# Optimization experiments

Hardware: AMD Instinct MI355X
Metric: run time of the kernel (lower is better)

The kernel has to match this reference:

```python
import jax, jax.numpy as jnp
import numpy as np

N_HEADS = 12
NEG_INF = -1e9


def rotate_half(x):
    x1, x2 = jnp.split(x, 2, axis=-1)
    return jnp.concatenate((-x2, x1), axis=-1)


def rope_tables(T, D, dtype):
    # matches RotaryEmbedding buffers: emb = cat(freqs, freqs), shape [1,1,T,D]
    inv_freq = 1.0 / (10000.0 ** (jnp.arange(0, D, 2, dtype=jnp.float32) / D))
    t = jnp.arange(T, dtype=jnp.float32)
    freqs = jnp.einsum('i,j->ij', t, inv_freq)
    emb = jnp.concatenate((freqs, freqs), axis=-1)
    return jnp.cos(emb)[None, None].astype(dtype), jnp.sin(emb)[None, None].astype(dtype)


def setup_inputs() -> dict:
    key = jax.random.key(0)
    ks = jax.random.split(key, 5)
    B, T, C = 4, 2048, 768
    s = 1.0 / np.sqrt(C)
    x = jax.random.normal(ks[0], (B, T, C), dtype=jnp.float32)
    wq = jax.random.normal(ks[1], (C, C), dtype=jnp.float32) * s
    wk = jax.random.normal(ks[2], (C, C), dtype=jnp.float32) * s
    wv = jax.random.normal(ks[3], (C, C), dtype=jnp.float32) * s
    wo = jax.random.normal(ks[4], (C, C), dtype=jnp.float32) * s
    causal = jnp.tril(jnp.ones((T, T), dtype=bool))
    mask = jnp.where(causal, 0.0, NEG_INF).astype(jnp.float32)[None, None]
    return {"x": x, "wq": wq, "wk": wk, "wv": wv, "wo": wo, "mask": mask}


def reference(x, wq, wk, wv, wo, mask):
    B, T, C = x.shape
    H = N_HEADS
    D = C // H
    # QKV projections (no bias), reshape to [B,H,T,D]
    def proj(w):
        return (x @ w).reshape(B, T, H, D).transpose(0, 2, 1, 3)
    q, k, v = proj(wq), proj(wk), proj(wv)
    cos, sin = rope_tables(T, D, x.dtype)
    q = q * cos + rotate_half(q) * sin
    k = k * cos + rotate_half(k) * sin
    attn = jnp.einsum('bhqd,bhkd->bhqk', q, k) / jnp.sqrt(jnp.asarray(D, x.dtype))
    attn = attn + mask
    attn = jax.nn.softmax(attn, axis=-1)  # dropout = identity (eval mode)
    out = jnp.einsum('bhqk,bhkd->bhqd', attn, v)
    out = out.transpose(0, 2, 1, 3).reshape(B, T, C)
    return out @ wo
```

## Files before the change

### kernel.cpp

```cpp
#include <hip/hip_runtime.h>
#include <hip/hip_bf16.h>
#include <cmath>

typedef _Float16 f16x8 __attribute__((ext_vector_type(8)));
typedef float f32x4 __attribute__((ext_vector_type(4)));

#define T_SEQ 2048
#define C_DIM 768
#define H_NUM 12
#define NX (8192 * 768)
#define NW (768 * 768)

__device__ __forceinline__ unsigned short f2h(float f) {
    _Float16 h = (_Float16)f;
    return __builtin_bit_cast(unsigned short, h);
}

__device__ __forceinline__ float fexp2(float x) {
#if __has_builtin(__builtin_amdgcn_exp2f)
    return __builtin_amdgcn_exp2f(x);
#else
    return exp2f(x);
#endif
}

__device__ __forceinline__ unsigned int pkrtz(float a, float b) {
    auto r = __builtin_amdgcn_cvt_pkrtz(a, b);
    return __builtin_bit_cast(unsigned int, r);
}

__device__ __forceinline__ unsigned int permlo(unsigned int d0, unsigned int d1) {
#if __has_builtin(__builtin_amdgcn_perm)
    return __builtin_amdgcn_perm(d1, d0, 0x05040100u);
#else
    return (d0 & 0xffffu) | (d1 << 16);
#endif
}
__device__ __forceinline__ unsigned int permhi(unsigned int d0, unsigned int d1) {
#if __has_builtin(__builtin_amdgcn_perm)
    return __builtin_amdgcn_perm(d1, d0, 0x07060302u);
#else
    return (d0 >> 16) | (d1 & 0xffff0000u);
#endif
}

__device__ __forceinline__ void gld16(const unsigned short* g, unsigned short* l) {
    __builtin_amdgcn_global_load_lds(
        (const __attribute__((address_space(1))) unsigned int*)g,
        (__attribute__((address_space(3))) unsigned int*)l, 16, 0, 0);
}

__global__ __launch_bounds__(256)
void prep(const float* __restrict__ x,
          const float* __restrict__ w0, const float* __restrict__ w1,
          const float* __restrict__ w2, const float* __restrict__ w3,
          unsigned short* __restrict__ xb, unsigned short* __restrict__ wt) {
    __shared__ float T[64][65];
    const int pid = blockIdx.x;
    if (pid < 3072) {
        int cidx = pid * 256 + threadIdx.x;
        int row = cidx / 96;
        int cp = cidx - row * 96;
        int dchunk = row * 96 + (cp & ~3) + ((cp & 3) ^ (row & 3));
        const float* s = x + (size_t)cidx * 8;
        float4 v0 = *(const float4*)s, v1 = *(const float4*)(s + 4);
        ushort4 a, b;
        a.x = f2h(v0.x); a.y = f2h(v0.y); a.z = f2h(v0.z); a.w = f2h(v0.w);
        b.x = f2h(v1.x); b.y = f2h(v1.y); b.z = f2h(v1.z); b.w = f2h(v1.w);
        unsigned short* d = xb + (size_t)dchunk * 8;
        *(ushort4*)d = a;
        *(ushort4*)(d + 4) = b;
    } else {
        int t = pid - 3072;
        int z = t / 144, r = t - z * 144;
        int kx = r / 12, ny = r - kx * 12;
        const float* src = (z == 0) ? w0 : (z == 1) ? w1 : (z == 2) ? w2 : w3;
        unsigned short* dst = wt + (size_t)z * NW;
        const int k0 = kx * 64, n0 = ny * 64;
        const int tid = threadIdx.x;
        {
            int rowb = tid >> 4, c4 = (tid & 15) * 4;
#pragma unroll
            for (int i = 0; i < 4; ++i) {
                int row = rowb + i * 16;
                float4 v = *(const float4*)&src[(size_t)(k0 + row) * C_DIM + n0 + c4];
                T[row][c4] = v.x; T[row][c4 + 1] = v.y; T[row][c4 + 2] = v.z; T[row][c4 + 3] = v.w;
            }
        }
        __syncthreads();
        {
            int n = tid & 63, kseg = (tid >> 6) * 16;
            int n_glob = n0 + n;
            unsigned short tmp[16];
#pragma unroll
            for (int j = 0; j < 16; ++j) tmp[j] = f2h(T[kseg + j][n]);
            int base = k0 + (kseg & 32);
            int sub = (kseg >> 3) & 3;
            unsigned short* drow = dst + (size_t)n_glob * C_DIM + base;
            *(uint4*)&drow[(sub ^ (n_glob & 3)) << 3]       = *(uint4*)&tmp[0];
            *(uint4*)&drow[((sub + 1) ^ (n_glob & 3)) << 3] = *(uint4*)&tmp[8];
        }
    }
}

__global__ __launch_bounds__(256, 4)
void qkv_gemm(const unsigned short* __restrict__ xb,
              const unsigned short* __restrict__ wt,
              unsigned short* __restrict__ q_ws,
              unsigned short* __restrict__ k_ws,
              unsigned short* __restrict__ vt_ws) {
    const int pid = blockIdx.x;
    const int xcd = pid & 7, idx = pid >> 3;
    const int mloc = idx / 18, nw = idx - mloc * 18;
    const int which = nw % 3, nx = nw / 3;
    const unsigned short* W = wt + (size_t)which * NW;
    const int n0 = nx * 128, m0 = (xcd * 8 + mloc) * 128;

    __shared__ __align__(16) unsigned short As[8192];
    __shared__ __align__(16) unsigned short Bs[8192];

    const int tid = threadIdx.x, lane = tid & 63, w = tid >> 6;
    const int quad = lane >> 4, l16 = lane & 15;
    const int wm = (w >> 1) * 64, wn = (w & 1) * 64;

    f32x4 acc[4][4] = {};

    for (int k0 = 0; k0 < C_DIM; k0 += 64) {
        __syncthreads();
#pragma unroll
        for (int c = 0; c < 4; ++c) {
            int e = c * 256 + tid;
            int p = e >> 9, row = (e >> 2) & 127, ch = e & 3;
            int kc = k0 + p * 32 + ch * 8;
            gld16(xb + (size_t)(m0 + row) * C_DIM + kc, &As[e * 8]);
            gld16(W  + (size_t)(n0 + row) * C_DIM + kc, &Bs[e * 8]);
        }
        __syncthreads();
#pragma unroll
        for (int p = 0; p < 2; ++p) {
            f16x8 af[4], bf[4];
#pragma unroll
            for (int mt = 0; mt < 4; ++mt) {
                int r = wm + mt * 16 + l16;
                af[mt] = *(const f16x8*)&As[p * 4096 + r * 32 + ((quad ^ (r & 3)) << 3)];
            }
#pragma unroll
            for (int nt = 0; nt < 4; ++nt) {
                int r = wn + nt * 16 + l16;
                bf[nt] = *(const f16x8*)&Bs[p * 4096 + r * 32 + ((quad ^ (r & 3)) << 3)];
            }
#pragma unroll
            for (int mt = 0; mt < 4; ++mt)
#pragma unroll
                for (int nt = 0; nt < 4; ++nt)
                    acc[mt][nt] = __builtin_amdgcn_mfma_f32_16x16x32_f16(af[mt], bf[nt], acc[mt][nt], 0, 0, 0);
        }
    }

    const int head = nx * 2 + (w & 1);

    if (which < 2) {
        unsigned short* dst = (which == 0) ? q_ws : k_ws;
        const float qscale = 0.18033688011112042f;
#pragma unroll
        for (int ntp = 0; ntp < 2; ++ntp) {
            int d1 = ntp * 16 + l16;
            float invf = __expf(-0.28782313662425572f * (float)d1);
#pragma unroll
            for (int mt = 0; mt < 4; ++mt)
#pragma unroll
                for (int reg = 0; reg < 4; ++reg) {
                    int m = m0 + wm + mt * 16 + quad * 4 + reg;
                    int t = m & (T_SEQ - 1), bb = m >> 11;
                    float sn, cs;
                    __sincosf((float)t * invf, &sn, &cs);
                    float v1 = acc[mt][ntp][reg], v2 = acc[mt][ntp + 2][reg];
                    float o1 = v1 * cs - v2 * sn;
                    float o2 = v2 * cs + v1 * sn;
                    if (which == 0) { o1 *= qscale; o2 *= qscale; }
                    size_t o = ((size_t)(bb * H_NUM + head) * T_SEQ + t) * 64 + d1;
                    dst[o] = f2h(o1);
                    dst[o + 32] = f2h(o2);
                }
        }
    } else {
#pragma unroll
        for (int nt = 0; nt < 4; ++nt) {
            int d = nt * 16 + l16;
#pragma unroll
            for (int mt = 0; mt < 4; ++mt) {
                int m = m0 + wm + mt * 16 + quad * 4;
                int t = m & (T_SEQ - 1), bb = m >> 11;
                ushort4 pk;
                pk.x = f2h(acc[mt][nt][0]); pk.y = f2h(acc[mt][nt][1]);
                pk.z = f2h(acc[mt][nt][2]); pk.w = f2h(acc[mt][nt][3]);
                *(ushort4*)&vt_ws[((size_t)(bb * H_NUM + head) * 64 + d) * T_SEQ + t] = pk;
            }
        }
    }
}

__global__ __launch_bounds__(256, 3)
void flash_attn(const unsigned short* __restrict__ q_ws,
                const unsigned short* __restrict__ k_ws,
                const unsigned short* __restrict__ vt_ws,
                unsigned short* __restrict__ attn_out) {
    __shared__ __align__(16) unsigned short Kbuf[2][64 * 64];
    __shared__ __align__(16) unsigned short Vbuf[2][64 * 64];
    __shared__ __align__(16) unsigned int Ps32[4][16 * 64];

    const int pid = blockIdx.x;
    const int xcd = pid & 7, slot = pid >> 3;
    const int bh_l = slot >> 4;
    const int bh = xcd * 6 + bh_l;
    const int pr = (slot + 3 * bh_l) & 15;
    const int qa = pr, qb = 31 - pr;
    const int b = bh / H_NUM, h = bh % H_NUM;

    const int tid = threadIdx.x, lane = tid & 63, w = tid >> 6;
    const int quad = lane >> 4, l16 = lane & 15;
    const size_t base = (size_t)bh * (T_SEQ * 64);

    const unsigned short* qAp = q_ws + base + (size_t)(qa * 64 + w * 16 + l16) * 64 + quad * 8;
    f16x8 aqA0 = *(const f16x8*)(qAp);
    f16x8 aqA1 = *(const f16x8*)(qAp + 32);
    const unsigned short* qBp = q_ws + base + (size_t)(qb * 64 + w * 16 + l16) * 64 + quad * 8;
    f16x8 aqB0 = *(const f16x8*)(qBp);
    f16x8 aqB1 = *(const f16x8*)(qBp + 32);

    f32x4 accA[4] = {}, accB[4] = {};
    f32x4 laccA = {}, laccB = {};
    f16x8 onesf;
#pragma unroll
    for (int i = 0; i < 8; ++i) onesf[i] = (_Float16)1.0f;

    unsigned int* pw = &Ps32[w][0];

    const int r_in = lane >> 3;
    const int cpr = lane & 7;
    const int gch = (cpr ^ r_in) * 8;

#define DMA_KV(P, KT)                                                                  \
    {                                                                                  \
        _Pragma("unroll")                                                              \
        for (int j = 0; j < 2; ++j) {                                                  \
            int row = w * 16 + j * 8 + r_in;                                           \
            gld16(k_ws + base + (size_t)((KT) * 64 + row) * 64 + gch,                  \
                  &Kbuf[P][(w * 16 + j * 8) * 64]);                                    \
            gld16(vt_ws + base + (size_t)row * T_SEQ + (KT) * 64 + gch,                \
                  &Vbuf[P][(w * 16 + j * 8) * 64]);                                    \
        }                                                                              \
    }

    const int fo = (quad ^ (l16 & 7)) << 3;

    const int wg = (quad & 1) * 4;
    const int l16q = l16 >> 2, l16m = l16 & 3;
    const int s7 = l16 & 7;
    const int rA = l16 * 64;
    const int rp0a = rA + (((2 * quad) ^ s7) << 2);
    const int rp0b = rA + (((2 * quad + 1) ^ s7) << 2);

    DMA_KV(0, 0);
    for (int kt = 0; kt <= qb; ++kt) {
        const int cur = kt & 1;
        __syncthreads();
        if (kt < qb) DMA_KV(cur ^ 1, kt + 1);
        const int doA = (kt <= qa);

        f16x8 bk[4][2], bv[4][2];
#pragma unroll
        for (int nt = 0; nt < 4; ++nt) {
            const unsigned short* kr = &Kbuf[cur][(nt * 16 + l16) * 64 + fo];
            bk[nt][0] = *(const f16x8*)(kr);
            bk[nt][1] = *(const f16x8*)((const unsigned short*)((size_t)kr ^ 64));
            const unsigned short* vr = &Vbuf[cur][(nt * 16 + l16) * 64 + fo];
            bv[nt][0] = *(const f16x8*)(vr);
            bv[nt][1] = *(const f16x8*)((const unsigned short*)((size_t)vr ^ 64));
        }

        f32x4 sB[4] = {}, sA[4] = {};
        __builtin_amdgcn_s_setprio(1);
#pragma unroll
        for (int nt = 0; nt < 4; ++nt) {
            sB[nt] = __builtin_amdgcn_mfma_f32_16x16x32_f16(aqB0, bk[nt][0], sB[nt], 0, 0, 0);
            sB[nt] = __builtin_amdgcn_mfma_f32_16x16x32_f16(aqB1, bk[nt][1], sB[nt], 0, 0, 0);
        }
        if (doA) {
#pragma unroll
            for (int nt = 0; nt < 4; ++nt) {
                sA[nt] = __builtin_amdgcn_mfma_f32_16x16x32_f16(aqA0, bk[nt][0], sA[nt], 0, 0, 0);
                sA[nt] = __builtin_amdgcn_mfma_f32_16x16x32_f16(aqA1, bk[nt][1], sA[nt], 0, 0, 0);
            }
        }
        __builtin_amdgcn_s_setprio(0);
        if (kt == qb) {
#pragma unroll
            for (int nt = 0; nt < 4; ++nt)
#pragma unroll
                for (int reg = 0; reg < 4; ++reg)
                    if (nt * 16 + l16 > w * 16 + quad * 4 + reg) sB[nt][reg] = -1e30f;
        }
        if (kt == qa) {
#pragma unroll
            for (int nt = 0; nt < 4; ++nt)
#pragma unroll
                for (int reg = 0; reg < 4; ++reg)
                    if (nt * 16 + l16 > w * 16 + quad * 4 + reg) sA[nt][reg] = -1e30f;
        }

        if (doA) {
#pragma unroll
            for (int nt = 0; nt < 4; ++nt)
#pragma unroll
                for (int reg = 0; reg < 4; ++reg) {
                    float pB = fexp2(sB[nt][reg]);
                    float pA = fexp2(sA[nt][reg]);
                    pw[(quad * 4 + reg) * 64 + ((((nt * 4) | l16q) ^ (wg | reg)) << 2) + l16m] = pkrtz(pB, pA);
                }
        } else {
#pragma unroll
            for (int nt = 0; nt < 4; ++nt)
#pragma unroll
                for (int reg = 0; reg < 4; ++reg) {
                    float pB = fexp2(sB[nt][reg]);
                    pw[(quad * 4 + reg) * 64 + ((((nt * 4) | l16q) ^ (wg | reg)) << 2) + l16m] = pkrtz(pB, pB);
                }
        }

        uint4 c0 = *(const uint4*)(pw + rp0a);
        uint4 c1 = *(const uint4*)(pw + rp0b);
        uint4 c2 = *(const uint4*)(pw + rp0a + 32);
        uint4 c3 = *(const uint4*)(pw + rp0b + 32);

        uint4 lo0 = { permlo(c0.x, c0.y), permlo(c0.z, c0.w), permlo(c1.x, c1.y), permlo(c1.z, c1.w) };
        uint4 lo1 = { permlo(c2.x, c2.y), permlo(c2.z, c2.w), permlo(c3.x, c3.y), permlo(c3.z, c3.w) };
        f16x8 apB0 = __builtin_bit_cast(f16x8, lo0);
        f16x8 apB1 = __builtin_bit_cast(f16x8, lo1);
        __builtin_amdgcn_s_setprio(1);
#pragma unroll
        for (int nt = 0; nt < 4; ++nt) {
            accB[nt] = __builtin_amdgcn_mfma_f32_16x16x32_f16(apB0, bv[nt][0], accB[nt], 0, 0, 0);
            accB[nt] = __builtin_amdgcn_mfma_f32_16x16x32_f16(apB1, bv[nt][1], accB[nt], 0, 0, 0);
        }
        laccB = __builtin_amdgcn_mfma_f32_16x16x32_f16(apB0, onesf, laccB, 0, 0, 0);
        laccB = __builtin_amdgcn_mfma_f32_16x16x32_f16(apB1, onesf, laccB, 0, 0, 0);
        __builtin_amdgcn_s_setprio(0);
        if (doA) {
            uint4 hi0 = { permhi(c0.x, c0.y), permhi(c0.z, c0.w), permhi(c1.x, c1.y), permhi(c1.z, c1.w) };
            uint4 hi1 = { permhi(c2.x, c2.y), permhi(c2.z, c2.w), permhi(c3.x, c3.y), permhi(c3.z, c3.w) };
            f16x8 apA0 = __builtin_bit_cast(f16x8, hi0);
            f16x8 apA1 = __builtin_bit_cast(f16x8, hi1);
            __builtin_amdgcn_s_setprio(1);
#pragma unroll
            for (int nt = 0; nt < 4; ++nt) {
                accA[nt] = __builtin_amdgcn_mfma_f32_16x16x32_f16(apA0, bv[nt][0], accA[nt], 0, 0, 0);
                accA[nt] = __builtin_amdgcn_mfma_f32_16x16x32_f16(apA1, bv[nt][1], accA[nt], 0, 0, 0);
            }
            laccA = __builtin_amdgcn_mfma_f32_16x16x32_f16(apA0, onesf, laccA, 0, 0, 0);
            laccA = __builtin_amdgcn_mfma_f32_16x16x32_f16(apA1, onesf, laccA, 0, 0, 0);
            __builtin_amdgcn_s_setprio(0);
        }
    }
#undef DMA_KV

    float lB[4], lA[4];
#pragma unroll
    for (int reg = 0; reg < 4; ++reg) {
        lB[reg] = 1.0f / laccB[reg];
        lA[reg] = 1.0f / laccA[reg];
    }
#pragma unroll
    for (int nt = 0; nt < 4; ++nt)
#pragma unroll
        for (int reg = 0; reg < 4; ++reg) {
            int col = h * 64 + nt * 16 + l16;
            int tB = qb * 64 + w * 16 + quad * 4 + reg;
            attn_out[(size_t)(b * T_SEQ + tB) * C_DIM + col] = f2h(accB[nt][reg] * lB[reg]);
            int tA = qa * 64 + w * 16 + quad * 4 + reg;
            attn_out[(size_t)(b * T_SEQ + tA) * C_DIM + col] = f2h(accA[nt][reg] * lA[reg]);
        }
}

__global__ __launch_bounds__(256, 3)
void out_proj(const unsigned short* __restrict__ ab,
              const unsigned short* __restrict__ wt_o,
              float* __restrict__ out) {
    const int pid = blockIdx.x;
    const int xcd = pid & 7, idx = pid >> 3;
    const int mloc = idx / 6, nx = idx - mloc * 6;
    const int n0 = nx * 128, m0 = (xcd * 8 + mloc) * 128;

    __shared__ __align__(16) unsigned short As[8192];
    __shared__ __align__(16) unsigned short Bs[8192];

    const int tid = threadIdx.x, lane = tid & 63, w = tid >> 6;
    const int quad = lane >> 4, l16 = lane & 15;
    const int wm = (w >> 1) * 64, wn = (w & 1) * 64;

    f32x4 acc[4][4] = {};
    const int srow = tid >> 1, shalf = tid & 1;

    for (int k0 = 0; k0 < C_DIM; k0 += 64) {
        __syncthreads();
#pragma unroll
        for (int p = 0; p < 2; ++p) {
            const unsigned short* g = ab + (size_t)(m0 + srow) * C_DIM + k0 + p * 32 + shalf * 16;
            uint4 d0 = *(const uint4*)g;
            uint4 d1 = *(const uint4*)(g + 8);
            *(uint4*)&As[p * 4096 + srow * 32 + (((shalf * 2 + 0) ^ (srow & 3)) << 3)] = d0;
            *(uint4*)&As[p * 4096 + srow * 32 + (((shalf * 2 + 1) ^ (srow & 3)) << 3)] = d1;
        }
#pragma unroll
        for (int c = 0; c < 4; ++c) {
            int e = c * 256 + tid;
            int p = e >> 9, row = (e >> 2) & 127, ch = e & 3;
            gld16(wt_o + (size_t)(n0 + row) * C_DIM + k0 + p * 32 + ch * 8, &Bs[e * 8]);
        }
        __syncthreads();
#pragma unroll
        for (int p = 0; p < 2; ++p) {
            f16x8 af[4], bf[4];
#pragma unroll
            for (int mt = 0; mt < 4; ++mt) {
                int r = wm + mt * 16 + l16;
                af[mt] = *(const f16x8*)&As[p * 4096 + r * 32 + ((quad ^ (r & 3)) << 3)];
            }
#pragma unroll
            for (int nt = 0; nt < 4; ++nt) {
                int r = wn + nt * 16 + l16;
                bf[nt] = *(const f16x8*)&Bs[p * 4096 + r * 32 + ((quad ^ (r & 3)) << 3)];
            }
#pragma unroll
            for (int mt = 0; mt < 4; ++mt)
#pragma unroll
                for (int nt = 0; nt < 4; ++nt)
                    acc[mt][nt] = __builtin_amdgcn_mfma_f32_16x16x32_f16(af[mt], bf[nt], acc[mt][nt], 0, 0, 0);
        }
    }

#pragma unroll
    for (int mt = 0; mt < 4; ++mt)
#pragma unroll
        for (int nt = 0; nt < 4; ++nt)
#pragma unroll
            for (int reg = 0; reg < 4; ++reg) {
                int m = m0 + wm + mt * 16 + quad * 4 + reg;
                int n = n0 + wn + nt * 16 + l16;
                out[(size_t)m * C_DIM + n] = acc[mt][nt][reg];
            }
}

extern "C" void kernel_launch(void* const* d_in, const int* in_sizes, int n_in,
                              void* d_out, int out_size, void* d_ws, size_t ws_size,
                              hipStream_t stream) {
    const float* x  = (const float*)d_in[0];
    const float* wq = (const float*)d_in[1];
    const float* wk = (const float*)d_in[2];
    const float* wv = (const float*)d_in[3];
    const float* wo = (const float*)d_in[4];
    float* out = (float*)d_out;

    unsigned short* xb    = (unsigned short*)d_ws;
    unsigned short* wt    = xb + NX;
    unsigned short* q_ws  = wt + 4 * (size_t)NW;
    unsigned short* k_ws  = q_ws + NX;
    unsigned short* vt_ws = k_ws + NX;
    unsigned short* attn  = xb;

    prep<<<3648, 256, 0, stream>>>(x, wq, wk, wv, wo, xb, wt);
    qkv_gemm<<<1152, 256, 0, stream>>>(xb, wt, q_ws, k_ws, vt_ws);
    flash_attn<<<768, 256, 0, stream>>>(q_ws, k_ws, vt_ws, attn);
    out_proj<<<384, 256, 0, stream>>>(attn, wt + 3 * (size_t)NW, out);
}
```

Measured before the change: 222.3 us.

## Compute transposed scores so P stays in registers, removing LDS round-trip

The QK^T MFMA now swaps its operands to produce S^T, so each lane's exponentiated probabilities already sit in the B-operand layout a 16x16x16 MFMA needs for the PV product. This removes the per-wave LDS staging buffer for P, along with its writes, reads and perm repacking. The row-sum moves from ones-vector MFMAs to fdot2 accumulation plus cross-lane shuffles at the end. V fragments are now read from LDS with 8-byte loads inside the PV loop, and PV uses twice as many smaller MFMAs. The output is written with vectorized ushort4 stores.

New measurement: 213.5 us. -4.0%, faster.

```diff
diff --git a/kernel.cpp b/kernel.cpp
--- a/kernel.cpp
+++ b/kernel.cpp
@@ -3,7 +3,9 @@
 #include <cmath>
 
 typedef _Float16 f16x8 __attribute__((ext_vector_type(8)));
+typedef _Float16 f16x4 __attribute__((ext_vector_type(4)));
 typedef float f32x4 __attribute__((ext_vector_type(4)));
+using h2_t = decltype(__builtin_amdgcn_cvt_pkrtz(0.f, 0.f));
 
 #define T_SEQ 2048
 #define C_DIM 768
@@ -24,23 +26,18 @@
 #endif
 }
 
-__device__ __forceinline__ unsigned int pkrtz(float a, float b) {
-    auto r = __builtin_amdgcn_cvt_pkrtz(a, b);
-    return __builtin_bit_cast(unsigned int, r);
-}
-
-__device__ __forceinline__ unsigned int permlo(unsigned int d0, unsigned int d1) {
-#if __has_builtin(__builtin_amdgcn_perm)
-    return __builtin_amdgcn_perm(d1, d0, 0x05040100u);
+__device__ __forceinline__ f16x4 mk4(h2_t a, h2_t b) {
+    uint2 u;
+    u.x = __builtin_bit_cast(unsigned int, a);
+    u.y = __builtin_bit_cast(unsigned int, b);
+    return __builtin_bit_cast(f16x4, u);
+}
+
+__device__ __forceinline__ float dot2acc(h2_t d, h2_t o, float acc) {
+#if __has_builtin(__builtin_amdgcn_fdot2)
+    return __builtin_amdgcn_fdot2(d, o, acc, false);
 #else
-    return (d0 & 0xffffu) | (d1 << 16);
-#endif
-}
-__device__ __forceinline__ unsigned int permhi(unsigned int d0, unsigned int d1) {
-#if __has_builtin(__builtin_amdgcn_perm)
-    return __builtin_amdgcn_perm(d1, d0, 0x07060302u);
-#else
-    return (d0 >> 16) | (d1 & 0xffff0000u);
+    return acc + (float)d[0] + (float)d[1];
 #endif
 }
 
@@ -207,7 +204,6 @@
                 unsigned short* __restrict__ attn_out) {
     __shared__ __align__(16) unsigned short Kbuf[2][64 * 64];
     __shared__ __align__(16) unsigned short Vbuf[2][64 * 64];
-    __shared__ __align__(16) unsigned int Ps32[4][16 * 64];
 
     const int pid = blockIdx.x;
     const int xcd = pid & 7, slot = pid >> 3;
@@ -229,12 +225,8 @@
     f16x8 aqB1 = *(const f16x8*)(qBp + 32);
 
     f32x4 accA[4] = {}, accB[4] = {};
-    f32x4 laccA = {}, laccB = {};
-    f16x8 onesf;
-#pragma unroll
-    for (int i = 0; i < 8; ++i) onesf[i] = (_Float16)1.0f;
-
-    unsigned int* pw = &Ps32[w][0];
+    float laccA = 0.f, laccB = 0.f;
+    const h2_t ones2 = __builtin_amdgcn_cvt_pkrtz(1.f, 1.f);
 
     const int r_in = lane >> 3;
     const int cpr = lane & 7;
@@ -254,12 +246,11 @@
 
     const int fo = (quad ^ (l16 & 7)) << 3;
 
-    const int wg = (quad & 1) * 4;
-    const int l16q = l16 >> 2, l16m = l16 & 3;
-    const int s7 = l16 & 7;
-    const int rA = l16 * 64;
-    const int rp0a = rA + (((2 * quad) ^ s7) << 2);
-    const int rp0b = rA + (((2 * quad + 1) ^ s7) << 2);
+    const int q1 = quad >> 1, q0 = quad & 1, s7 = l16 & 7;
+    int voff[4];
+#pragma unroll
+    for (int kb = 0; kb < 4; ++kb)
+        voff[kb] = (((((kb << 1) | q1) ^ s7) << 3) | (q0 << 2));
 
     DMA_KV(0, 0);
     for (int kt = 0; kt <= qb; ++kt) {
@@ -268,118 +259,113 @@
         if (kt < qb) DMA_KV(cur ^ 1, kt + 1);
         const int doA = (kt <= qa);
 
-        f16x8 bk[4][2], bv[4][2];
+        f16x8 bk[4][2];
 #pragma unroll
         for (int nt = 0; nt < 4; ++nt) {
             const unsigned short* kr = &Kbuf[cur][(nt * 16 + l16) * 64 + fo];
             bk[nt][0] = *(const f16x8*)(kr);
             bk[nt][1] = *(const f16x8*)((const unsigned short*)((size_t)kr ^ 64));
-            const unsigned short* vr = &Vbuf[cur][(nt * 16 + l16) * 64 + fo];
-            bv[nt][0] = *(const f16x8*)(vr);
-            bv[nt][1] = *(const f16x8*)((const unsigned short*)((size_t)vr ^ 64));
         }
 
         f32x4 sB[4] = {}, sA[4] = {};
         __builtin_amdgcn_s_setprio(1);
 #pragma unroll
         for (int nt = 0; nt < 4; ++nt) {
-            sB[nt] = __builtin_amdgcn_mfma_f32_16x16x32_f16(aqB0, bk[nt][0], sB[nt], 0, 0, 0);
-            sB[nt] = __builtin_amdgcn_mfma_f32_16x16x32_f16(aqB1, bk[nt][1], sB[nt], 0, 0, 0);
+            sB[nt] = __builtin_amdgcn_mfma_f32_16x16x32_f16(bk[nt][0], aqB0, sB[nt], 0, 0, 0);
+            sB[nt] = __builtin_amdgcn_mfma_f32_16x16x32_f16(bk[nt][1], aqB1, sB[nt], 0, 0, 0);
         }
         if (doA) {
 #pragma unroll
             for (int nt = 0; nt < 4; ++nt) {
-                sA[nt] = __builtin_amdgcn_mfma_f32_16x16x32_f16(aqA0, bk[nt][0], sA[nt], 0, 0, 0);
-                sA[nt] = __builtin_amdgcn_mfma_f32_16x16x32_f16(aqA1, bk[nt][1], sA[nt], 0, 0, 0);
+                sA[nt] = __builtin_amdgcn_mfma_f32_16x16x32_f16(bk[nt][0], aqA0, sA[nt], 0, 0, 0);
+                sA[nt] = __builtin_amdgcn_mfma_f32_16x16x32_f16(bk[nt][1], aqA1, sA[nt], 0, 0, 0);
             }
         }
         __builtin_amdgcn_s_setprio(0);
+
         if (kt == qb) {
 #pragma unroll
             for (int nt = 0; nt < 4; ++nt)
 #pragma unroll
                 for (int reg = 0; reg < 4; ++reg)
-                    if (nt * 16 + l16 > w * 16 + quad * 4 + reg) sB[nt][reg] = -1e30f;
+                    if (nt * 16 + quad * 4 + reg > w * 16 + l16) sB[nt][reg] = -1e30f;
         }
         if (kt == qa) {
 #pragma unroll
             for (int nt = 0; nt < 4; ++nt)
 #pragma unroll
                 for (int reg = 0; reg < 4; ++reg)
-                    if (nt * 16 + l16 > w * 16 + quad * 4 + reg) sA[nt][reg] = -1e30f;
-        }
-
+                    if (nt * 16 + quad * 4 + reg > w * 16 + l16) sA[nt][reg] = -1e30f;
+        }
+
+        f16x4 pbB[4], pbA[4];
+#pragma unroll
+        for (int kb = 0; kb < 4; ++kb) {
+            float p0 = fexp2(sB[kb][0]), p1 = fexp2(sB[kb][1]);
+            float p2 = fexp2(sB[kb][2]), p3 = fexp2(sB[kb][3]);
+            h2_t d0 = __builtin_amdgcn_cvt_pkrtz(p0, p1);
+            h2_t d1 = __builtin_amdgcn_cvt_pkrtz(p2, p3);
+            laccB = dot2acc(d0, ones2, laccB);
+            laccB = dot2acc(d1, ones2, laccB);
+            pbB[kb] = mk4(d0, d1);
+        }
         if (doA) {
 #pragma unroll
-            for (int nt = 0; nt < 4; ++nt)
-#pragma unroll
-                for (int reg = 0; reg < 4; ++reg) {
-                    float pB = fexp2(sB[nt][reg]);
-                    float pA = fexp2(sA[nt][reg]);
-                    pw[(quad * 4 + reg) * 64 + ((((nt * 4) | l16q) ^ (wg | reg)) << 2) + l16m] = pkrtz(pB, pA);
-                }
-        } else {
-#pragma unroll
-            for (int nt = 0; nt < 4; ++nt)
-#pragma unroll
-                for (int reg = 0; reg < 4; ++reg) {
-                    float pB = fexp2(sB[nt][reg]);
-                    pw[(quad * 4 + reg) * 64 + ((((nt * 4) | l16q) ^ (wg | reg)) << 2) + l16m] = pkrtz(pB, pB);
-                }
-        }
-
-        uint4 c0 = *(const uint4*)(pw + rp0a);
-        uint4 c1 = *(const uint4*)(pw + rp0b);
-        uint4 c2 = *(const uint4*)(pw + rp0a + 32);
-        uint4 c3 = *(const uint4*)(pw + rp0b + 32);
-
-        uint4 lo0 = { permlo(c0.x, c0.y), permlo(c0.z, c0.w), permlo(c1.x, c1.y), permlo(c1.z, c1.w) };
-        uint4 lo1 = { permlo(c2.x, c2.y), permlo(c2.z, c2.w), permlo(c3.x, c3.y), permlo(c3.z, c3.w) };
-        f16x8 apB0 = __builtin_bit_cast(f16x8, lo0);
-        f16x8 apB1 = __builtin_bit_cast(f16x8, lo1);
+            for (int kb = 0; kb < 4; ++kb) {
+                float p0 = fexp2(sA[kb][0]), p1 = fexp2(sA[kb][1]);
+                float p2 = fexp2(sA[kb][2]), p3 = fexp2(sA[kb][3]);
+                h2_t d0 = __builtin_amdgcn_cvt_pkrtz(p0, p1);
+                h2_t d1 = __builtin_amdgcn_cvt_pkrtz(p2, p3);
+                laccA = dot2acc(d0, ones2, laccA);
+                laccA = dot2acc(d1, ones2, laccA);
+                pbA[kb] = mk4(d0, d1);
+            }
+        }
+
         __builtin_amdgcn_s_setprio(1);
 #pragma unroll
-        for (int nt = 0; nt < 4; ++nt) {
-            accB[nt] = __builtin_amdgcn_mfma_f32_16x16x32_f16(apB0, bv[nt][0], accB[nt], 0, 0, 0);
-            accB[nt] = __builtin_amdgcn_mfma_f32_16x16x32_f16(apB1, bv[nt][1], accB[nt], 0, 0, 0);
-        }
-        laccB = __builtin_amdgcn_mfma_f32_16x16x32_f16(apB0, onesf, laccB, 0, 0, 0);
-        laccB = __builtin_amdgcn_mfma_f32_16x16x32_f16(apB1, onesf, laccB, 0, 0, 0);
+        for (int ntd = 0; ntd < 4; ++ntd) {
+            const unsigned short* vrow = &Vbuf[cur][(ntd * 16 + l16) * 64];
+            f16x4 av0 = *(const f16x4*)(vrow + voff[0]);
+            f16x4 av1 = *(const f16x4*)(vrow + voff[1]);
+            f16x4 av2 = *(const f16x4*)(vrow + voff[2]);
+            f16x4 av3 = *(const f16x4*)(vrow + voff[3]);
+            accB[ntd] = __builtin_amdgcn_mfma_f32_16x16x16f16(av0, pbB[0], accB[ntd], 0, 0, 0);
+            accB[ntd] = __builtin_amdgcn_mfma_f32_16x16x16f16(av1, pbB[1], accB[ntd], 0, 0, 0);
+            accB[ntd] = __builtin_amdgcn_mfma_f32_16x16x16f16(av2, pbB[2], accB[ntd], 0, 0, 0);
+            accB[ntd] = __builtin_amdgcn_mfma_f32_16x16x16f16(av3, pbB[3], accB[ntd], 0, 0, 0);
+            if (doA) {
+                accA[ntd] = __builtin_amdgcn_mfma_f32_16x16x16f16(av0, pbA[0], accA[ntd], 0, 0, 0);
+                accA[ntd] = __builtin_amdgcn_mfma_f32_16x16x16f16(av1, pbA[1], accA[ntd], 0, 0, 0);
+                accA[ntd] = __builtin_amdgcn_mfma_f32_16x16x16f16(av2, pbA[2], accA[ntd], 0, 0, 0);
+                accA[ntd] = __builtin_amdgcn_mfma_f32_16x16x16f16(av3, pbA[3], accA[ntd], 0, 0, 0);
+            }
+        }
         __builtin_amdgcn_s_setprio(0);
-        if (doA) {
-            uint4 hi0 = { permhi(c0.x, c0.y), permhi(c0.z, c0.w), permhi(c1.x, c1.y), permhi(c1.z, c1.w) };
-            uint4 hi1 = { permhi(c2.x, c2.y), permhi(c2.z, c2.w), permhi(c3.x, c3.y), permhi(c3.z, c3.w) };
-            f16x8 apA0 = __builtin_bit_cast(f16x8, hi0);
-            f16x8 apA1 = __builtin_bit_cast(f16x8, hi1);
-            __builtin_amdgcn_s_setprio(1);
-#pragma unroll
-            for (int nt = 0; nt < 4; ++nt) {
-                accA[nt] = __builtin_amdgcn_mfma_f32_16x16x32_f16(apA0, bv[nt][0], accA[nt], 0, 0, 0);
-                accA[nt] = __builtin_amdgcn_mfma_f32_16x16x32_f16(apA1, bv[nt][1], accA[nt], 0, 0, 0);
-            }
-            laccA = __builtin_amdgcn_mfma_f32_16x16x32_f16(apA0, onesf, laccA, 0, 0, 0);
-            laccA = __builtin_amdgcn_mfma_f32_16x16x32_f16(apA1, onesf, laccA, 0, 0, 0);
-            __builtin_amdgcn_s_setprio(0);
-        }
     }
 #undef DMA_KV
 
-    float lB[4], lA[4];
-#pragma unroll
-    for (int reg = 0; reg < 4; ++reg) {
-        lB[reg] = 1.0f / laccB[reg];
-        lA[reg] = 1.0f / laccA[reg];
-    }
-#pragma unroll
-    for (int nt = 0; nt < 4; ++nt)
-#pragma unroll
-        for (int reg = 0; reg < 4; ++reg) {
-            int col = h * 64 + nt * 16 + l16;
-            int tB = qb * 64 + w * 16 + quad * 4 + reg;
-            attn_out[(size_t)(b * T_SEQ + tB) * C_DIM + col] = f2h(accB[nt][reg] * lB[reg]);
-            int tA = qa * 64 + w * 16 + quad * 4 + reg;
-            attn_out[(size_t)(b * T_SEQ + tA) * C_DIM + col] = f2h(accA[nt][reg] * lA[reg]);
-        }
+    laccB += __shfl_xor(laccB, 16);
+    laccB += __shfl_xor(laccB, 32);
+    laccA += __shfl_xor(laccA, 16);
+    laccA += __shfl_xor(laccA, 32);
+    const float rB = 1.0f / laccB;
+    const float rA = 1.0f / laccA;
+
+    const int tB = qb * 64 + w * 16 + l16;
+    const int tA = qa * 64 + w * 16 + l16;
+#pragma unroll
+    for (int ntd = 0; ntd < 4; ++ntd) {
+        int col = h * 64 + ntd * 16 + quad * 4;
+        ushort4 pkB;
+        pkB.x = f2h(accB[ntd][0] * rB); pkB.y = f2h(accB[ntd][1] * rB);
+        pkB.z = f2h(accB[ntd][2] * rB); pkB.w = f2h(accB[ntd][3] * rB);
+        *(ushort4*)&attn_out[(size_t)(b * T_SEQ + tB) * C_DIM + col] = pkB;
+        ushort4 pkA;
+        pkA.x = f2h(accA[ntd][0] * rA); pkA.y = f2h(accA[ntd][1] * rA);
+        pkA.z = f2h(accA[ntd][2] * rA); pkA.w = f2h(accA[ntd][3] * rA);
+        *(ushort4*)&attn_out[(size_t)(b * T_SEQ + tA) * C_DIM + col] = pkA;
+    }
 }
 
 __global__ __launch_bounds__(256, 3)
```
